# Kernel tuning notes

Hardware: AMD Instinct MI355X
Metric: run time of the kernel (lower is better)

## Reference

```python
import jax, jax.numpy as jnp
import numpy as np

N_NODES = 50000
N_EDGES = 800000
F_IN = 128
HEADS = 4
HEAD_DIM = 32  # hidden_size // heads
HIDDEN = HEADS * HEAD_DIM
N_GRAPHS = 64
LEAKY_SLOPE = 0.01
EPS_LN = 1e-5


def setup_inputs() -> dict:
    key = jax.random.key(0)
    ks = jax.random.split(key, 12)
    x = jax.random.normal(ks[0], (N_NODES, F_IN), dtype=jnp.float32)
    edge_index = jax.random.randint(ks[1], (2, N_EDGES), 0, N_NODES, dtype=jnp.int64)
    batch = jnp.sort(jax.random.randint(ks[2], (N_NODES,), 0, N_GRAPHS, dtype=jnp.int64))
    s = 1.0 / np.sqrt(F_IN).astype(np.float32)
    Wq = jax.random.normal(ks[3], (F_IN, HIDDEN), dtype=jnp.float32) * s
    bq = jnp.zeros((HIDDEN,), jnp.float32)
    Wk = jax.random.normal(ks[4], (F_IN, HIDDEN), dtype=jnp.float32) * s
    bk = jnp.zeros((HIDDEN,), jnp.float32)
    Wv = jax.random.normal(ks[5], (F_IN, HIDDEN), dtype=jnp.float32) * s
    bv = jnp.zeros((HIDDEN,), jnp.float32)
    Ws = jax.random.normal(ks[6], (F_IN, HIDDEN), dtype=jnp.float32) * s  # root/skip lin
    bs = jnp.zeros((HIDDEN,), jnp.float32)
    ln_w = jnp.ones((HIDDEN,), jnp.float32)
    ln_b = jnp.zeros((HIDDEN,), jnp.float32)
    return {"x": x, "edge_index": edge_index, "batch": batch,
            "Wq": Wq, "bq": bq, "Wk": Wk, "bk": bk, "Wv": Wv, "bv": bv,
            "Ws": Ws, "bs": bs, "ln_w": ln_w, "ln_b": ln_b}


def reference(x, edge_index, batch, Wq, bq, Wk, bk, Wv, bv, Ws, bs, ln_w, ln_b):
    N = x.shape[0]
    src, dst = edge_index[0], edge_index[1]  # message j(src) -> i(dst)
    q = (x @ Wq + bq).reshape(N, HEADS, HEAD_DIM)
    k = (x @ Wk + bk).reshape(N, HEADS, HEAD_DIM)
    v = (x @ Wv + bv).reshape(N, HEADS, HEAD_DIM)
    # per-edge attention logits [E, H]
    alpha = jnp.einsum('ehc,ehc->eh', q[dst], k[src]) / jnp.sqrt(jnp.float32(HEAD_DIM))
    # scatter-softmax over incoming edges of each destination node
    m = jax.ops.segment_max(alpha, dst, num_segments=N)
    m = jnp.where(jnp.isfinite(m), m, 0.0)  # empty segments -> -inf; neutralize
    ex = jnp.exp(alpha - m[dst])
    denom = jax.ops.segment_sum(ex, dst, num_segments=N)
    attn = ex / (denom[dst] + 1e-16)
    # scatter-add aggregation of weighted values, concat heads
    out = jax.ops.segment_sum(attn[:, :, None] * v[src], dst, num_segments=N)
    out = out.reshape(N, HIDDEN) + x @ Ws + bs  # root/skip connection
    # PyG graph-mode LayerNorm: normalize over all nodes+channels of each graph
    cnt = jax.ops.segment_sum(jnp.ones((N,), out.dtype), batch, num_segments=N_GRAPHS)
    norm = jnp.maximum(cnt, 1.0) * HIDDEN
    mean = jax.ops.segment_sum(out.sum(-1), batch, num_segments=N_GRAPHS) / norm
    outc = out - mean[batch][:, None]
    var = jax.ops.segment_sum((outc * outc).sum(-1), batch, num_segments=N_GRAPHS) / norm
    y = outc / jnp.sqrt(var + EPS_LN)[batch][:, None]
    y = y * ln_w + ln_b
    y = jnp.where(y > 0, y, LEAKY_SLOPE * y)  # LeakyReLU
    return (y, attn)
```

## Files before the change

### kernel.cpp

```cpp
#include <hip/hip_runtime.h>
#include <hip/hip_fp16.h>

constexpr int N_NODES = 50000;
constexpr int N_EDGES = 800000;
constexpr int HIDDEN  = 128;
constexpr float RSQRT_D = 0.17677669529663687f;
constexpr int Y_SIZE = N_NODES * HIDDEN;
constexpr int M_PAD  = 50048;
constexpr int SCAN_BLOCKS = 196;
constexpr int XCVT_BLOCKS = (M_PAD * 16) / 256;
constexpr int HIST_BLOCKS = N_EDGES / 256;
constexpr int STAT_BLOCKS = (N_NODES + 31) / 32;

constexpr size_t OFF_Q      = 0;
constexpr size_t OFF_K      = 6400000;
constexpr size_t OFF_S      = 19200000;
constexpr size_t OFF_EXC    = 22400000;
constexpr size_t OFF_WT     = 25600000;
constexpr size_t OFF_GSUM   = 25800000;
constexpr size_t OFF_GSQ    = 25800064;
constexpr size_t OFF_GCNT   = 25800128;
constexpr size_t OFF_DEG    = 25800192;
constexpr size_t OFF_OFFS   = 25850192;
constexpr size_t OFF_CURSOR = 25900224;
constexpr size_t OFF_CSR    = 25950224;
constexpr size_t OFF_PART   = 27550224;

typedef __attribute__((ext_vector_type(8))) short bf16x8;
typedef __attribute__((ext_vector_type(4))) float f32x4;

__device__ __forceinline__ short f2bf(float f) {
    unsigned u = __float_as_uint(f);
    unsigned r = (u + 0x7fff + ((u >> 16) & 1)) >> 16;
    return (short)r;
}

__device__ __forceinline__ void gload_lds16(const void* g, void* l) {
    __builtin_amdgcn_global_load_lds(
        (const __attribute__((address_space(1))) void*)g,
        (__attribute__((address_space(3))) void*)l, 16, 0, 0);
}

__global__ __launch_bounds__(256) void k_prep(
    const float* __restrict__ x,
    const float* __restrict__ Wq, const float* __restrict__ Wk,
    const float* __restrict__ Wv, const float* __restrict__ Wsm,
    const int* __restrict__ dst,
    short* __restrict__ xs, short* __restrict__ wt, int* __restrict__ deg)
{
    int b = blockIdx.x;
    if (b < XCVT_BLOCKS) {
        int tid = b * 256 + threadIdx.x;
        int row = tid >> 4, ci = tid & 15;
        short o[8];
        if (row < N_NODES) {
            float4 a = *(const float4*)&x[(size_t)row * 128 + ci * 8];
            float4 bb = *(const float4*)&x[(size_t)row * 128 + ci * 8 + 4];
            o[0] = f2bf(a.x); o[1] = f2bf(a.y); o[2] = f2bf(a.z); o[3] = f2bf(a.w);
            o[4] = f2bf(bb.x); o[5] = f2bf(bb.y); o[6] = f2bf(bb.z); o[7] = f2bf(bb.w);
        } else {
            #pragma unroll
            for (int j = 0; j < 8; ++j) o[j] = 0;
        }
        int cs = ci ^ (row & 7);
        *(int4*)&xs[(size_t)row * 128 + cs * 8] = *(int4*)o;
    } else if (b < XCVT_BLOCKS + 32) {
        int tid = (b - XCVT_BLOCKS) * 256 + threadIdx.x;
        int mat = tid >> 11, n = (tid >> 4) & 127, kg = tid & 15;
        const float* W = (mat == 0) ? Wq : (mat == 1) ? Wk : (mat == 2) ? Wv : Wsm;
        short o[8];
        #pragma unroll
        for (int j = 0; j < 8; ++j) o[j] = f2bf(W[(kg * 8 + j) * 128 + n]);
        int cs = kg ^ (n & 7);
        *(int4*)&wt[mat * 16384 + n * 128 + cs * 8] = *(int4*)o;
    } else {
        int e = (b - XCVT_BLOCKS - 32) * 256 + threadIdx.x;
        atomicAdd(&deg[dst[e]], 1);
    }
}

__global__ __launch_bounds__(256) void k_mm(
    const short* __restrict__ xs, const short* __restrict__ wt,
    const float* __restrict__ bq, const float* __restrict__ bk,
    const float* __restrict__ bv, const float* __restrict__ bs,
    __half* __restrict__ qb, __half* __restrict__ kv, __half* __restrict__ sb)
{
    __shared__ __align__(16) char As[32768];
    __shared__ __align__(16) char Bs[32768];
    const int t = threadIdx.x, lane = t & 63, wv = t >> 6;
    const int m0 = blockIdx.x * 128;
    const int wm = wv >> 1, wn = wv & 1;

    const char* gA = (const char*)xs + (size_t)m0 * 256;
    #pragma unroll
    for (int i = 0; i < 8; ++i) {
        int chunk = wv * 8 + i;
        gload_lds16(gA + chunk * 1024 + lane * 16, As + chunk * 1024);
        gload_lds16((const char*)wt + chunk * 1024 + lane * 16, Bs + chunk * 1024);
    }
    __syncthreads();

    bf16x8 af[4][4];
    #pragma unroll
    for (int ks = 0; ks < 4; ++ks) {
        const int cbase = ks * 64 + ((lane >> 4) << 4);
        #pragma unroll
        for (int mf = 0; mf < 4; ++mf) {
            int mr = wm * 64 + mf * 16 + (lane & 15);
            af[ks][mf] = *(const bf16x8*)(As + mr * 256 + (cbase ^ ((mr & 7) << 4)));
        }
    }

    const float* Bbs[4] = {bq, bk, bv, bs};
    #pragma unroll
    for (int mat = 0; mat < 4; ++mat) {
        f32x4 acc[4][4];
        #pragma unroll
        for (int nf = 0; nf < 4; ++nf) {
            float bc = Bbs[mat][wn * 64 + nf * 16 + (lane & 15)];
            #pragma unroll
            for (int mf = 0; mf < 4; ++mf) acc[mf][nf] = (f32x4){bc, bc, bc, bc};
        }
        #pragma unroll
        for (int ks = 0; ks < 4; ++ks) {
            bf16x8 bfr[4];
            const int cbase = ks * 64 + ((lane >> 4) << 4);
            #pragma unroll
            for (int nf = 0; nf < 4; ++nf) {
                int nc = wn * 64 + nf * 16 + (lane & 15);
                bfr[nf] = *(const bf16x8*)(Bs + nc * 256 + (cbase ^ ((nc & 7) << 4)));
            }
            #pragma unroll
            for (int mf = 0; mf < 4; ++mf)
                #pragma unroll
                for (int nf = 0; nf < 4; ++nf)
                    acc[mf][nf] = __builtin_amdgcn_mfma_f32_16x16x32_bf16(
                        af[ks][mf], bfr[nf], acc[mf][nf], 0, 0, 0);
        }
        __syncthreads();
        if (mat < 3) {
            const char* gB = (const char*)wt + (mat + 1) * 32768;
            #pragma unroll
            for (int i = 0; i < 8; ++i) {
                int chunk = wv * 8 + i;
                gload_lds16(gB + chunk * 1024 + lane * 16, Bs + chunk * 1024);
            }
        }
        __half* base = (mat == 0) ? qb : (mat == 1) ? kv : (mat == 2) ? (kv + 128) : sb;
        const int rs = (mat == 1 || mat == 2) ? 256 : 128;
        const int colbase = wn * 64 + (lane & 15);
        #pragma unroll
        for (int mf = 0; mf < 4; ++mf) {
            int rowb = m0 + wm * 64 + mf * 16 + ((lane >> 4) << 2);
            #pragma unroll
            for (int nf = 0; nf < 4; ++nf) {
                int col = colbase + nf * 16;
                #pragma unroll
                for (int r = 0; r < 4; ++r) {
                    int node = rowb + r;
                    if (node < N_NODES)
                        base[(size_t)node * rs + col] = __float2half_rn(acc[mf][nf][r]);
                }
            }
        }
        __syncthreads();
    }
}

__global__ __launch_bounds__(256) void k_scan1(const int* __restrict__ deg,
                                               int* __restrict__ part)
{
    const int t = threadIdx.x;
    int idx = blockIdx.x * 256 + t;
    int v = (idx < N_NODES) ? deg[idx] : 0;
    #pragma unroll
    for (int o = 1; o < 64; o <<= 1) v += __shfl_xor(v, o);
    __shared__ int wsum[4];
    if ((t & 63) == 0) wsum[t >> 6] = v;
    __syncthreads();
    if (t == 0) part[blockIdx.x] = wsum[0] + wsum[1] + wsum[2] + wsum[3];
}

__global__ __launch_bounds__(256) void k_scan3(const int* __restrict__ deg,
                                               const int* __restrict__ part,
                                               int* __restrict__ offs,
                                               int* __restrict__ cursor)
{
    __shared__ int pbuf[256];
    __shared__ int wsum[4];
    const int t = threadIdx.x;
    int pv = (t < SCAN_BLOCKS) ? part[t] : 0;
    pbuf[t] = pv;
    __syncthreads();
    for (int o = 1; o < 256; o <<= 1) {
        int tmp = (t >= o) ? pbuf[t - o] : 0;
        __syncthreads();
        pbuf[t] += tmp;
        __syncthreads();
    }
    const int bbase = (blockIdx.x == 0) ? 0 : pbuf[blockIdx.x - 1];

    const int idx = blockIdx.x * 256 + t;
    const int lane = t & 63, w = t >> 6;
    int v = (idx < N_NODES) ? deg[idx] : 0;
    int inc = v;
    #pragma unroll
    for (int o = 1; o < 64; o <<= 1) {
        int nb = __shfl_up(inc, o);
        if (lane >= o) inc += nb;
    }
    if (lane == 63) wsum[w] = inc;
    __syncthreads();
    int wbase = 0;
    #pragma unroll
    for (int i = 0; i < 4; ++i) if (i < w) wbase += wsum[i];
    int excl = bbase + wbase + inc - v;
    if (idx < N_NODES) {
        offs[idx] = excl;
        cursor[idx] = excl;
    }
    if (idx == 0) offs[N_NODES] = N_EDGES;
}

__global__ __launch_bounds__(256) void k_scatter(
    const int* __restrict__ src, const int* __restrict__ dst,
    int* __restrict__ cursor, int2* __restrict__ csr)
{
    int e = blockIdx.x * 256 + threadIdx.x;
    int d = dst[e];
    int p = atomicAdd(&cursor[d], 1);
    csr[p] = make_int2(src[e], e);
}

__global__ __launch_bounds__(256) void k_fused(
    const __half* __restrict__ qb, const __half* __restrict__ kv,
    const __half* __restrict__ sb,
    const int* __restrict__ offs, const int2* __restrict__ csr,
    float* __restrict__ exc, float* __restrict__ attn,
    float* __restrict__ outb)
{
    const int t = threadIdx.x;
    const int lane = t & 63;
    const int n = blockIdx.x * 4 + (t >> 6);
    const int begin = offs[n], end = offs[n + 1];
    const int cl  = lane & 15;
    const int qtr = lane >> 4;
    const int h   = cl >> 2;

    const __half2* qp = (const __half2*)(qb + (size_t)n * 128 + cl * 8);
    float2 qf[4];
    #pragma unroll
    for (int j = 0; j < 4; ++j) qf[j] = __half22float2(qp[j]);

    float acc[8] = {0.f, 0.f, 0.f, 0.f, 0.f, 0.f, 0.f, 0.f};
    float dsum = 0.f;
    int i = begin;
    for (; i + 8 <= end; i += 8) {
        const int s0 = csr[i + qtr].x;
        const int s1 = csr[i + 4 + qtr].x;
        const __half2* k0 = (const __half2*)(kv + (size_t)s0 * 256 + cl * 8);
        const __half2* k1 = (const __half2*)(kv + (size_t)s1 * 256 + cl * 8);
        __half2 ka[4], kb2[4], va[4], vb2[4];
        #pragma unroll
        for (int j = 0; j < 4; ++j) { ka[j] = k0[j]; va[j] = k0[64 + j]; }
        #pragma unroll
        for (int j = 0; j < 4; ++j) { kb2[j] = k1[j]; vb2[j] = k1[64 + j]; }
        float p0 = 0.f, p1 = 0.f;
        #pragma unroll
        for (int j = 0; j < 4; ++j) {
            float2 f0 = __half22float2(ka[j]), f1 = __half22float2(kb2[j]);
            p0 += qf[j].x * f0.x + qf[j].y * f0.y;
            p1 += qf[j].x * f1.x + qf[j].y * f1.y;
        }
        p0 += __shfl_xor(p0, 1);  p1 += __shfl_xor(p1, 1);
        p0 += __shfl_xor(p0, 2);  p1 += __shfl_xor(p1, 2);
        const float ex0 = __expf(p0 * RSQRT_D);
        const float ex1 = __expf(p1 * RSQRT_D);
        dsum += ex0 + ex1;
        #pragma unroll
        for (int j = 0; j < 4; ++j) {
            float2 f0 = __half22float2(va[j]), f1 = __half22float2(vb2[j]);
            acc[2*j]   += ex0 * f0.x + ex1 * f1.x;
            acc[2*j+1] += ex0 * f0.y + ex1 * f1.y;
        }
        if ((lane & 3) == 0) {
            exc[(i + qtr) * 4 + h]     = ex0;
            exc[(i + 4 + qtr) * 4 + h] = ex1;
        }
    }
    for (; i < end; i += 4) {
        const int eIdx = i + qtr;
        const bool act = eIdx < end;
        const int s0 = csr[act ? eIdx : end - 1].x;
        const __half2* k0 = (const __half2*)(kv + (size_t)s0 * 256 + cl * 8);
        __half2 ka[4], va[4];
        #pragma unroll
        for (int j = 0; j < 4; ++j) { ka[j] = k0[j]; va[j] = k0[64 + j]; }
        float p0 = 0.f;
        #pragma unroll
        for (int j = 0; j < 4; ++j) {
            float2 f0 = __half22float2(ka[j]);
            p0 += qf[j].x * f0.x + qf[j].y * f0.y;
        }
        p0 += __shfl_xor(p0, 1);
        p0 += __shfl_xor(p0, 2);
        const float ex0 = act ? __expf(p0 * RSQRT_D) : 0.f;
        dsum += ex0;
        #pragma unroll
        for (int j = 0; j < 4; ++j) {
            float2 f0 = __half22float2(va[j]);
            acc[2*j]   += ex0 * f0.x;
            acc[2*j+1] += ex0 * f0.y;
        }
        if (((lane & 3) == 0) && act) exc[eIdx * 4 + h] = ex0;
    }
    dsum += __shfl_xor(dsum, 16);
    dsum += __shfl_xor(dsum, 32);
    #pragma unroll
    for (int j = 0; j < 8; ++j) {
        acc[j] += __shfl_xor(acc[j], 16);
        acc[j] += __shfl_xor(acc[j], 32);
    }
    const float rd0 = 1.f / (__shfl(dsum, 0)  + 1e-16f);
    const float rd1 = 1.f / (__shfl(dsum, 4)  + 1e-16f);
    const float rd2 = 1.f / (__shfl(dsum, 8)  + 1e-16f);
    const float rd3 = 1.f / (__shfl(dsum, 12) + 1e-16f);

    if (lane < 16) {
        const float rdn = 1.f / (dsum + 1e-16f);
        const __half2* sp = (const __half2*)(sb + (size_t)n * 128 + cl * 8);
        float o[8];
        #pragma unroll
        for (int j = 0; j < 4; ++j) {
            float2 sf = __half22float2(sp[j]);
            o[2*j]   = acc[2*j]   * rdn + sf.x;
            o[2*j+1] = acc[2*j+1] * rdn + sf.y;
        }
        *(float4*)&outb[(size_t)n * 128 + cl * 8]     = make_float4(o[0], o[1], o[2], o[3]);
        *(float4*)&outb[(size_t)n * 128 + cl * 8 + 4] = make_float4(o[4], o[5], o[6], o[7]);
    }

    for (int slot = begin + lane; slot < end; slot += 64) {
        const int eid = csr[slot].y;
        float4 e4 = *(const float4*)&exc[slot * 4];
        ((float4*)attn)[eid] = make_float4(e4.x * rd0, e4.y * rd1,
                                           e4.z * rd2, e4.w * rd3);
    }
}

__global__ __launch_bounds__(256) void k_stats(
    const float* __restrict__ out, const int* __restrict__ batch,
    float* __restrict__ gsum, float* __restrict__ gsq, int* __restrict__ gcnt)
{
    __shared__ float nsum[32], nsq[32];
    __shared__ int   ngr[32];
    const int t = threadIdx.x;
    const int nl = t >> 3, part = t & 7;
    const int n = blockIdx.x * 32 + nl;
    float lsum = 0.f, lsq = 0.f;
    if (n < N_NODES) {
        size_t base = (size_t)n * 128 + part * 16;
        #pragma unroll
        for (int i = 0; i < 4; ++i) {
            float4 o = *(const float4*)&out[base + i * 4];
            lsum += o.x + o.y + o.z + o.w;
            lsq  += o.x * o.x + o.y * o.y + o.z * o.z + o.w * o.w;
        }
    }
    #pragma unroll
    for (int o = 1; o < 8; o <<= 1) {
        lsum += __shfl_xor(lsum, o);
        lsq  += __shfl_xor(lsq, o);
    }
    if (part == 0) { nsum[nl] = lsum; nsq[nl] = lsq; ngr[nl] = (n < N_NODES) ? batch[n] : -1; }
    __syncthreads();
    if (t == 0) {
        float acc = 0.f, accq = 0.f; int cg = ngr[0], cnt = 0;
        for (int i = 0; i < 32; ++i) {
            int g = ngr[i];
            if (g != cg) {
                if (cg >= 0) { atomicAdd(&gsum[cg], acc); atomicAdd(&gsq[cg], accq);
                               atomicAdd(&gcnt[cg], cnt); }
                acc = 0.f; accq = 0.f; cnt = 0; cg = g;
            }
            acc += nsum[i]; accq += nsq[i]; ++cnt;
        }
        if (cg >= 0) { atomicAdd(&gsum[cg], acc); atomicAdd(&gsq[cg], accq);
                       atomicAdd(&gcnt[cg], cnt); }
    }
}

__global__ __launch_bounds__(256) void k_final(
    const float* __restrict__ out, const int* __restrict__ batch,
    const float* __restrict__ gsum, const float* __restrict__ gsq,
    const int* __restrict__ gcnt,
    const float* __restrict__ lnw, const float* __restrict__ lnb,
    float* __restrict__ y)
{
    int idx = blockIdx.x * 256 + threadIdx.x;
    int n = idx >> 7, c = idx & 127;
    int g = batch[n];
    float norm = fmaxf((float)gcnt[g], 1.f) * 128.f;
    float mean = gsum[g] / norm;
    float var  = gsq[g] / norm - mean * mean;
    float inv  = rsqrtf(var + 1e-5f);
    float val  = (out[idx] - mean) * inv * lnw[c] + lnb[c];
    y[idx] = val > 0.f ? val : 0.01f * val;
}

extern "C" void kernel_launch(void* const* d_in, const int* in_sizes, int n_in,
                              void* d_out, int out_size, void* d_ws, size_t ws_size,
                              hipStream_t stream)
{
    (void)in_sizes; (void)n_in; (void)out_size; (void)ws_size;
    const float* x    = (const float*)d_in[0];
    const int*   ei   = (const int*)  d_in[1];
    const int*   batch= (const int*)  d_in[2];
    const float* Wq   = (const float*)d_in[3];
    const float* bq   = (const float*)d_in[4];
    const float* Wk   = (const float*)d_in[5];
    const float* bk   = (const float*)d_in[6];
    const float* Wv   = (const float*)d_in[7];
    const float* bv   = (const float*)d_in[8];
    const float* Wsm  = (const float*)d_in[9];
    const float* bs   = (const float*)d_in[10];
    const float* lnw  = (const float*)d_in[11];
    const float* lnb  = (const float*)d_in[12];

    float* outp = (float*)d_out;
    float* ws   = (float*)d_ws;

    const int* srcI = ei;
    const int* dstI = ei + N_EDGES;

    __half* qb      = (__half*)(ws + OFF_Q);
    __half* kv      = (__half*)(ws + OFF_K);
    __half* sb      = (__half*)(ws + OFF_S);
    float*  exc     = ws + OFF_EXC;
    short*  wt      = (short*)(ws + OFF_WT);
    float*  gsum    = ws + OFF_GSUM;
    float*  gsq     = ws + OFF_GSQ;
    int*    gcnt    = (int*)(ws + OFF_GCNT);
    int*    deg     = (int*)(ws + OFF_DEG);
    int*    offs    = (int*)(ws + OFF_OFFS);
    int*    cursor  = (int*)(ws + OFF_CURSOR);
    int2*   csr     = (int2*)(ws + OFF_CSR);
    int*    partArr = (int*)(ws + OFF_PART);

    float* outb  = outp;
    short* x_swz = (short*)outp;
    float* attn  = outp + Y_SIZE;

    hipMemsetAsync(gsum, 0, (size_t)(192 + N_NODES) * sizeof(float), stream);

    k_prep<<<XCVT_BLOCKS + 32 + HIST_BLOCKS, 256, 0, stream>>>(
        x, Wq, Wk, Wv, Wsm, dstI, x_swz, wt, deg);
    k_mm<<<M_PAD / 128, 256, 0, stream>>>(x_swz, wt, bq, bk, bv, bs, qb, kv, sb);

    k_scan1<<<SCAN_BLOCKS, 256, 0, stream>>>(deg, partArr);
    k_scan3<<<SCAN_BLOCKS, 256, 0, stream>>>(deg, partArr, offs, cursor);
    k_scatter<<<N_EDGES / 256, 256, 0, stream>>>(srcI, dstI, cursor, csr);
    k_fused<<<N_NODES / 4, 256, 0, stream>>>(qb, kv, sb, offs, csr,
                                             exc, attn, outb);
    k_stats<<<STAT_BLOCKS, 256, 0, stream>>>(outb, batch, gsum, gsq, gcnt);
    k_final<<<Y_SIZE / 256, 256, 0, stream>>>(outb, batch, gsum, gsq, gcnt,
                                              lnw, lnb, outp);
}
```

Before: 227.2 us.

## Merge scan1 into matmul launch, prefetch edge gathers, stage exp scores in LDS

Folds the degree-partial-sum kernel into the matmul launch as extra blocks, removing one kernel launch. In the fused attention kernel, the loop now software-pipelines one group of four edges, loading the next group's K/V rows while computing the current one. Per-edge exp values for the first 128 incoming edges of each node go to shared memory instead of a global scratch buffer, so the normalisation pass avoids a global round trip. The trade-offs are more live registers and 8 KB of LDS per block, which can lower occupancy, plus a sched_barrier that limits instruction reordering.

Measured after the change: 228.0 us. About the same (+0.4%).

```diff
diff --git a/kernel.cpp b/kernel.cpp
--- a/kernel.cpp
+++ b/kernel.cpp
@@ -7,10 +7,12 @@
 constexpr float RSQRT_D = 0.17677669529663687f;
 constexpr int Y_SIZE = N_NODES * HIDDEN;
 constexpr int M_PAD  = 50048;
+constexpr int MM_BLOCKS = M_PAD / 128;
 constexpr int SCAN_BLOCKS = 196;
 constexpr int XCVT_BLOCKS = (M_PAD * 16) / 256;
 constexpr int HIST_BLOCKS = N_EDGES / 256;
 constexpr int STAT_BLOCKS = (N_NODES + 31) / 32;
+constexpr int EX_CAP = 128;
 
 constexpr size_t OFF_Q      = 0;
 constexpr size_t OFF_K      = 6400000;
@@ -79,12 +81,25 @@
     }
 }
 
-__global__ __launch_bounds__(256) void k_mm(
+__global__ __launch_bounds__(256) void k_mmscan(
     const short* __restrict__ xs, const short* __restrict__ wt,
     const float* __restrict__ bq, const float* __restrict__ bk,
     const float* __restrict__ bv, const float* __restrict__ bs,
-    __half* __restrict__ qb, __half* __restrict__ kv, __half* __restrict__ sb)
-{
+    __half* __restrict__ qb, __half* __restrict__ kv, __half* __restrict__ sb,
+    const int* __restrict__ deg, int* __restrict__ part)
+{
+    if (blockIdx.x >= MM_BLOCKS) {
+        const int t = threadIdx.x;
+        int idx = (blockIdx.x - MM_BLOCKS) * 256 + t;
+        int v = (idx < N_NODES) ? deg[idx] : 0;
+        #pragma unroll
+        for (int o = 1; o < 64; o <<= 1) v += __shfl_xor(v, o);
+        __shared__ int wsum1[4];
+        if ((t & 63) == 0) wsum1[t >> 6] = v;
+        __syncthreads();
+        if (t == 0) part[blockIdx.x - MM_BLOCKS] = wsum1[0] + wsum1[1] + wsum1[2] + wsum1[3];
+        return;
+    }
     __shared__ __align__(16) char As[32768];
     __shared__ __align__(16) char Bs[32768];
     const int t = threadIdx.x, lane = t & 63, wv = t >> 6;
@@ -165,20 +180,6 @@
         }
         __syncthreads();
     }
-}
-
-__global__ __launch_bounds__(256) void k_scan1(const int* __restrict__ deg,
-                                               int* __restrict__ part)
-{
-    const int t = threadIdx.x;
-    int idx = blockIdx.x * 256 + t;
-    int v = (idx < N_NODES) ? deg[idx] : 0;
-    #pragma unroll
-    for (int o = 1; o < 64; o <<= 1) v += __shfl_xor(v, o);
-    __shared__ int wsum[4];
-    if ((t & 63) == 0) wsum[t >> 6] = v;
-    __syncthreads();
-    if (t == 0) part[blockIdx.x] = wsum[0] + wsum[1] + wsum[2] + wsum[3];
 }
 
 __global__ __launch_bounds__(256) void k_scan3(const int* __restrict__ deg,
@@ -232,6 +233,29 @@
     csr[p] = make_int2(src[e], e);
 }
 
+#define GRP_COMPUTE(BASE, K0, K1, K2, K3, V0, V1, V2, V3)                     \
+    {                                                                         \
+        float2 f0 = __half22float2(K0), f1 = __half22float2(K1),              \
+               f2 = __half22float2(K2), f3 = __half22float2(K3);              \
+        float p = qf[0].x*f0.x + qf[0].y*f0.y + qf[1].x*f1.x + qf[1].y*f1.y   \
+                + qf[2].x*f2.x + qf[2].y*f2.y + qf[3].x*f3.x + qf[3].y*f3.y;  \
+        p += __shfl_xor(p, 1);                                                \
+        p += __shfl_xor(p, 2);                                                \
+        const float ex = __expf(p * RSQRT_D);                                 \
+        dsum += ex;                                                           \
+        float2 g0 = __half22float2(V0), g1 = __half22float2(V1),              \
+               g2 = __half22float2(V2), g3 = __half22float2(V3);              \
+        acc[0] += ex * g0.x; acc[1] += ex * g0.y;                             \
+        acc[2] += ex * g1.x; acc[3] += ex * g1.y;                             \
+        acc[4] += ex * g2.x; acc[5] += ex * g2.y;                             \
+        acc[6] += ex * g3.x; acc[7] += ex * g3.y;                             \
+        if ((lane & 3) == 0) {                                                \
+            int sl = (BASE) + qtr - begin;                                    \
+            if (sl < EX_CAP) exs[nl][sl * 4 + h] = ex;                        \
+            else             exc[((size_t)((BASE) + qtr)) * 4 + h] = ex;      \
+        }                                                                     \
+    }
+
 __global__ __launch_bounds__(256) void k_fused(
     const __half* __restrict__ qb, const __half* __restrict__ kv,
     const __half* __restrict__ sb,
@@ -239,9 +263,11 @@
     float* __restrict__ exc, float* __restrict__ attn,
     float* __restrict__ outb)
 {
+    __shared__ __align__(16) float exs[4][EX_CAP * 4];
     const int t = threadIdx.x;
     const int lane = t & 63;
-    const int n = blockIdx.x * 4 + (t >> 6);
+    const int nl = t >> 6;
+    const int n = blockIdx.x * 4 + nl;
     const int begin = offs[n], end = offs[n + 1];
     const int cl  = lane & 15;
     const int qtr = lane >> 4;
@@ -255,65 +281,50 @@
     float acc[8] = {0.f, 0.f, 0.f, 0.f, 0.f, 0.f, 0.f, 0.f};
     float dsum = 0.f;
     int i = begin;
-    for (; i + 8 <= end; i += 8) {
-        const int s0 = csr[i + qtr].x;
-        const int s1 = csr[i + 4 + qtr].x;
-        const __half2* k0 = (const __half2*)(kv + (size_t)s0 * 256 + cl * 8);
-        const __half2* k1 = (const __half2*)(kv + (size_t)s1 * 256 + cl * 8);
-        __half2 ka[4], kb2[4], va[4], vb2[4];
-        #pragma unroll
-        for (int j = 0; j < 4; ++j) { ka[j] = k0[j]; va[j] = k0[64 + j]; }
-        #pragma unroll
-        for (int j = 0; j < 4; ++j) { kb2[j] = k1[j]; vb2[j] = k1[64 + j]; }
-        float p0 = 0.f, p1 = 0.f;
-        #pragma unroll
-        for (int j = 0; j < 4; ++j) {
-            float2 f0 = __half22float2(ka[j]), f1 = __half22float2(kb2[j]);
-            p0 += qf[j].x * f0.x + qf[j].y * f0.y;
-            p1 += qf[j].x * f1.x + qf[j].y * f1.y;
-        }
-        p0 += __shfl_xor(p0, 1);  p1 += __shfl_xor(p1, 1);
-        p0 += __shfl_xor(p0, 2);  p1 += __shfl_xor(p1, 2);
-        const float ex0 = __expf(p0 * RSQRT_D);
-        const float ex1 = __expf(p1 * RSQRT_D);
-        dsum += ex0 + ex1;
-        #pragma unroll
-        for (int j = 0; j < 4; ++j) {
-            float2 f0 = __half22float2(va[j]), f1 = __half22float2(vb2[j]);
-            acc[2*j]   += ex0 * f0.x + ex1 * f1.x;
-            acc[2*j+1] += ex0 * f0.y + ex1 * f1.y;
-        }
-        if ((lane & 3) == 0) {
-            exc[(i + qtr) * 4 + h]     = ex0;
-            exc[(i + 4 + qtr) * 4 + h] = ex1;
-        }
-    }
-    for (; i < end; i += 4) {
+
+    if (i + 4 <= end) {
+        const __half2* kpC = (const __half2*)(kv + (size_t)csr[i + qtr].x * 256 + cl * 8);
+        __half2 kC0 = kpC[0],  kC1 = kpC[1],  kC2 = kpC[2],  kC3 = kpC[3];
+        __half2 vC0 = kpC[64], vC1 = kpC[65], vC2 = kpC[66], vC3 = kpC[67];
+        while (i + 8 <= end) {
+            const __half2* kpN = (const __half2*)(kv + (size_t)csr[i + 4 + qtr].x * 256 + cl * 8);
+            __half2 kN0 = kpN[0],  kN1 = kpN[1],  kN2 = kpN[2],  kN3 = kpN[3];
+            __half2 vN0 = kpN[64], vN1 = kpN[65], vN2 = kpN[66], vN3 = kpN[67];
+            GRP_COMPUTE(i, kC0, kC1, kC2, kC3, vC0, vC1, vC2, vC3);
+            kC0 = kN0; kC1 = kN1; kC2 = kN2; kC3 = kN3;
+            vC0 = vN0; vC1 = vN1; vC2 = vN2; vC3 = vN3;
+            i += 4;
+        }
+        GRP_COMPUTE(i, kC0, kC1, kC2, kC3, vC0, vC1, vC2, vC3);
+        i += 4;
+    }
+    if (i < end) {
         const int eIdx = i + qtr;
         const bool act = eIdx < end;
-        const int s0 = csr[act ? eIdx : end - 1].x;
-        const __half2* k0 = (const __half2*)(kv + (size_t)s0 * 256 + cl * 8);
-        __half2 ka[4], va[4];
-        #pragma unroll
-        for (int j = 0; j < 4; ++j) { ka[j] = k0[j]; va[j] = k0[64 + j]; }
-        float p0 = 0.f;
-        #pragma unroll
-        for (int j = 0; j < 4; ++j) {
-            float2 f0 = __half22float2(ka[j]);
-            p0 += qf[j].x * f0.x + qf[j].y * f0.y;
-        }
-        p0 += __shfl_xor(p0, 1);
-        p0 += __shfl_xor(p0, 2);
-        const float ex0 = act ? __expf(p0 * RSQRT_D) : 0.f;
-        dsum += ex0;
-        #pragma unroll
-        for (int j = 0; j < 4; ++j) {
-            float2 f0 = __half22float2(va[j]);
-            acc[2*j]   += ex0 * f0.x;
-            acc[2*j+1] += ex0 * f0.y;
-        }
-        if (((lane & 3) == 0) && act) exc[eIdx * 4 + h] = ex0;
-    }
+        const __half2* kp = (const __half2*)(kv + (size_t)csr[act ? eIdx : end - 1].x * 256 + cl * 8);
+        __half2 ka0 = kp[0],  ka1 = kp[1],  ka2 = kp[2],  ka3 = kp[3];
+        __half2 va0 = kp[64], va1 = kp[65], va2 = kp[66], va3 = kp[67];
+        float2 f0 = __half22float2(ka0), f1 = __half22float2(ka1),
+               f2 = __half22float2(ka2), f3 = __half22float2(ka3);
+        float p = qf[0].x*f0.x + qf[0].y*f0.y + qf[1].x*f1.x + qf[1].y*f1.y
+                + qf[2].x*f2.x + qf[2].y*f2.y + qf[3].x*f3.x + qf[3].y*f3.y;
+        p += __shfl_xor(p, 1);
+        p += __shfl_xor(p, 2);
+        const float ex = act ? __expf(p * RSQRT_D) : 0.f;
+        dsum += ex;
+        float2 g0 = __half22float2(va0), g1 = __half22float2(va1),
+               g2 = __half22float2(va2), g3 = __half22float2(va3);
+        acc[0] += ex * g0.x; acc[1] += ex * g0.y;
+        acc[2] += ex * g1.x; acc[3] += ex * g1.y;
+        acc[4] += ex * g2.x; acc[5] += ex * g2.y;
+        acc[6] += ex * g3.x; acc[7] += ex * g3.y;
+        if (((lane & 3) == 0) && act) {
+            int sl = eIdx - begin;
+            if (sl < EX_CAP) exs[nl][sl * 4 + h] = ex;
+            else             exc[(size_t)eIdx * 4 + h] = ex;
+        }
+    }
+
     dsum += __shfl_xor(dsum, 16);
     dsum += __shfl_xor(dsum, 32);
     #pragma unroll
@@ -340,9 +351,13 @@
         *(float4*)&outb[(size_t)n * 128 + cl * 8 + 4] = make_float4(o[4], o[5], o[6], o[7]);
     }
 
+    __builtin_amdgcn_sched_barrier(0);
+
     for (int slot = begin + lane; slot < end; slot += 64) {
         const int eid = csr[slot].y;
-        float4 e4 = *(const float4*)&exc[slot * 4];
+        const int sl = slot - begin;
+        float4 e4 = (sl < EX_CAP) ? *(const float4*)&exs[nl][sl * 4]
+                                  : *(const float4*)&exc[(size_t)slot * 4];
         ((float4*)attn)[eid] = make_float4(e4.x * rd0, e4.y * rd1,
                                            e4.z * rd2, e4.w * rd3);
     }
@@ -455,9 +470,8 @@
 
     k_prep<<<XCVT_BLOCKS + 32 + HIST_BLOCKS, 256, 0, stream>>>(
         x, Wq, Wk, Wv, Wsm, dstI, x_swz, wt, deg);
-    k_mm<<<M_PAD / 128, 256, 0, stream>>>(x_swz, wt, bq, bk, bv, bs, qb, kv, sb);
-
-    k_scan1<<<SCAN_BLOCKS, 256, 0, stream>>>(deg, partArr);
+    k_mmscan<<<MM_BLOCKS + SCAN_BLOCKS, 256, 0, stream>>>(
+        x_swz, wt, bq, bk, bv, bs, qb, kv, sb, deg, partArr);
     k_scan3<<<SCAN_BLOCKS, 256, 0, stream>>>(deg, partArr, offs, cursor);
     k_scatter<<<N_EDGES / 256, 256, 0, stream>>>(srcI, dstI, cursor, csr);
     k_fused<<<N_NODES / 4, 256, 0, stream>>>(qb, kv, sb, offs, csr,
```
